# Kernel optimization log

Measured on AMD Instinct MI355X. Metric: run time of the kernel, lower is better.

Reference implementation:

```python
import jax, jax.numpy as jnp
import numpy as np
import math

B, T, D = 2, 2048, 1024
H, DH = 16, 64  # n_heads, d_head
ROPE_THETA = 10000.0


def _rope_cos_sin(seq_len, d_head, dtype):
    # inv_freq over even indices, freqs[i,j] = t_i * inv_freq_j, shape [T, d_head//2]
    inv_freq = 1.0 / (ROPE_THETA ** (jnp.arange(0, d_head, 2, dtype=jnp.float32) / d_head))
    freqs = jnp.arange(seq_len, dtype=jnp.float32)[:, None] * inv_freq[None, :]
    # emb = cat(freqs, freqs); we only ever index cos[..., :d_head//2], so keep the half
    cos = jnp.cos(freqs).astype(dtype)[None, :, None, :]  # [1,T,1,DH/2]
    sin = jnp.sin(freqs).astype(dtype)[None, :, None, :]
    return cos, sin


def _apply_rotation(x, cos, sin):
    # x: [B,T,H,DH]; rotate-half style as in the torch module
    x1, x2 = x[..., : x.shape[-1] // 2], x[..., x.shape[-1] // 2 :]
    return jnp.concatenate([x1 * cos - x2 * sin, x1 * sin + x2 * cos], axis=-1)


def setup_inputs() -> dict:
    key = jax.random.key(0)
    k1, k2, k3 = jax.random.split(key, 3)
    x = jax.random.normal(k1, (B, T, D), dtype=jnp.float32)
    # torch Linear weights stored transposed here as [in, out]; init_std=0.02
    Wqkv = jax.random.normal(k2, (D, 3 * D), dtype=jnp.float32) * 0.02
    Wout = jax.random.normal(k3, (D, D), dtype=jnp.float32) * 0.02
    return {"x": x, "Wqkv": Wqkv, "Wout": Wout}


def reference(x, Wqkv, Wout):
    b, t, d = x.shape
    qkv = x @ Wqkv  # [B,T,3D]
    q, k, v = jnp.split(qkv, 3, axis=-1)
    q = q.reshape(b, t, H, DH)
    k = k.reshape(b, t, H, DH)
    v = v.reshape(b, t, H, DH)

    cos, sin = _rope_cos_sin(t, DH, x.dtype)
    q = _apply_rotation(q, cos, sin)
    k = _apply_rotation(k, cos, sin)

    scale = 1.0 / math.sqrt(DH)
    # scores: [B,H,Tq,Tk]
    scores = jnp.einsum("bqhd,bkhd->bhqk", q, k) * scale
    causal = jnp.triu(jnp.ones((t, t), dtype=bool), k=1)
    scores = jnp.where(causal[None, None, :, :], -jnp.inf, scores)
    attn = jax.nn.softmax(scores, axis=-1)
    # dropout in eval mode -> identity
    out = jnp.einsum("bhqk,bkhd->bqhd", attn, v).reshape(b, t, d)
    return out @ Wout
```

## Files before the change

kernel.cpp:

```cpp
#include <hip/hip_runtime.h>
#include <hip/hip_bf16.h>
#include <stdint.h>
#include <math.h>

#define T_SEQ 2048
#define NHEAD 16
#define NBH   32
#define BTROW 4096

typedef __bf16 bf16_t;
typedef __bf16 bf16x4_t __attribute__((ext_vector_type(4)));
typedef __bf16 bf16x8_t __attribute__((ext_vector_type(8)));
typedef float  f32x4_t  __attribute__((ext_vector_type(4)));

#define QSCALE 0.18033688011112042f

__device__ __forceinline__ f32x4_t mfma16(bf16x8_t a, bf16x8_t b, f32x4_t c) {
  return __builtin_amdgcn_mfma_f32_16x16x32_bf16(a, b, c, 0, 0, 0);
}

__device__ __forceinline__ float fast_exp2(float x) {
#if __has_builtin(__builtin_amdgcn_exp2f)
  return __builtin_amdgcn_exp2f(x);
#else
  return exp2f(x);
#endif
}

__device__ __forceinline__ void gl_lds16(const bf16_t* g, bf16_t* l) {
  __builtin_amdgcn_global_load_lds(
      (const __attribute__((address_space(1))) void*)g,
      (__attribute__((address_space(3))) void*)l, 16, 0, 0);
}

__global__ __launch_bounds__(256) void k_cast_bf16(const float* __restrict__ in,
                                                   bf16_t* __restrict__ out, int n) {
  int tid = blockIdx.x * blockDim.x + threadIdx.x;
  int stride = gridDim.x * blockDim.x;
  for (int i = tid * 4; i < n; i += stride * 4) {
    float4 a = *(const float4*)(in + i);
    bf16x4_t r = { (bf16_t)a.x, (bf16_t)a.y, (bf16_t)a.z, (bf16_t)a.w };
    *(bf16x4_t*)(out + i) = r;
  }
}

__global__ __launch_bounds__(256) void k_trans_cast(const float* __restrict__ W,
                                                    bf16_t* __restrict__ WT,
                                                    int K, int N) {
  __shared__ float tile[32][33];
  int n0 = blockIdx.x * 32, k0 = blockIdx.y * 32;
  int tx = threadIdx.x & 31, ty = threadIdx.x >> 5;
#pragma unroll
  for (int j = 0; j < 4; j++)
    tile[ty + j * 8][tx] = W[(size_t)(k0 + ty + j * 8) * N + n0 + tx];
  __syncthreads();
#pragma unroll
  for (int j = 0; j < 4; j++)
    WT[(size_t)(n0 + ty + j * 8) * K + k0 + tx] = (bf16_t)tile[tx][ty + j * 8];
}

__global__ __launch_bounds__(256) void k_rope_table(float* __restrict__ cs,
                                                    float* __restrict__ sn) {
  int i = blockIdx.x * blockDim.x + threadIdx.x;
  if (i >= T_SEQ * 32) return;
  int t = i >> 5, j = i & 31;
  float inv = powf(10000.0f, -(float)(2 * j) / 64.0f);
  float f = (float)t * inv;
  cs[i] = cosf(f);
  sn[i] = sinf(f);
}

__global__ __launch_bounds__(256) void k_gemm_qkv(const bf16_t* __restrict__ A,
                                                  const bf16_t* __restrict__ Bt,
                                                  const float* __restrict__ cs,
                                                  const float* __restrict__ sn,
                                                  bf16_t* __restrict__ Qr,
                                                  bf16_t* __restrict__ Kr,
                                                  bf16_t* __restrict__ Vt) {
  const int K = 1024;
  __shared__ __align__(16) unsigned char smem[128 * 132 * 2];
  bf16_t* As = (bf16_t*)smem;
  bf16_t* Bs = (bf16_t*)(smem + 8192);
  bf16_t* vtile = (bf16_t*)smem;

  int m0 = blockIdx.y * 128, n0 = blockIdx.x * 128;
  int tid = threadIdx.x;
  int lane = tid & 63, w = tid >> 6;
  int wr = w >> 1, wc = w & 1;
  int l15 = lane & 15, l4 = lane >> 4;

  f32x4_t acc[4][4];
#pragma unroll
  for (int m = 0; m < 4; m++)
#pragma unroll
    for (int n = 0; n < 4; n++) acc[m][n] = (f32x4_t){0.f, 0.f, 0.f, 0.f};

  for (int k0 = 0; k0 < K; k0 += 32) {
#pragma unroll
    for (int j = 0; j < 2; j++) {
      int c = j * 256 + tid;
      int row = c >> 2, kb = c & 3;
      gl_lds16(A + (size_t)(m0 + row) * K + k0 + kb * 8, As + (size_t)(j * 256 + w * 64) * 8);
      gl_lds16(Bt + (size_t)(n0 + row) * K + k0 + kb * 8, Bs + (size_t)(j * 256 + w * 64) * 8);
    }
    __syncthreads();
    bf16x8_t af[4], bfr[4];
#pragma unroll
    for (int m = 0; m < 4; m++)
      af[m] = *(const bf16x8_t*)(As + (size_t)(wr * 64 + m * 16 + l15) * 32 + l4 * 8);
#pragma unroll
    for (int n = 0; n < 4; n++)
      bfr[n] = *(const bf16x8_t*)(Bs + (size_t)(wc * 64 + n * 16 + l15) * 32 + l4 * 8);
#pragma unroll
    for (int m = 0; m < 4; m++)
#pragma unroll
      for (int n = 0; n < 4; n++) acc[m][n] = mfma16(af[m], bfr[n], acc[m][n]);
    __syncthreads();
  }

  int region = n0 >> 10;
  if (region < 2) {
    bf16_t* dst = region ? Kr : Qr;
    float qs = region ? 1.0f : QSCALE;
    int h = ((n0 & 1023) + wc * 64) >> 6;
#pragma unroll
    for (int m = 0; m < 4; m++)
#pragma unroll
      for (int r = 0; r < 4; r++) {
        int row = m0 + wr * 64 + m * 16 + l4 * 4 + r;
        int b = row >> 11, t = row & 2047;
        size_t obase = ((size_t)(b * NHEAD + h) * T_SEQ + t) * 64;
#pragma unroll
        for (int n = 0; n < 2; n++) {
          int j = n * 16 + l15;
          float c = cs[t * 32 + j], s = sn[t * 32 + j];
          float x1 = acc[m][n][r], x2 = acc[m][n + 2][r];
          dst[obase + j]      = (bf16_t)((x1 * c - x2 * s) * qs);
          dst[obase + 32 + j] = (bf16_t)((x1 * s + x2 * c) * qs);
        }
      }
  } else {
#pragma unroll
    for (int m = 0; m < 4; m++)
#pragma unroll
      for (int n = 0; n < 4; n++)
#pragma unroll
        for (int r = 0; r < 4; r++)
          vtile[(size_t)(wc * 64 + n * 16 + l15) * 132 + wr * 64 + m * 16 + l4 * 4 + r] =
              (bf16_t)acc[m][n][r];
    __syncthreads();
    int colbase = n0 - 2048;
    int b = m0 >> 11, t0l = m0 & 2047;
#pragma unroll
    for (int p = 0; p < 64; p++) {
      int idx = p * 256 + tid;
      int dl = idx >> 7, tl = idx & 127;
      int col = colbase + dl, h = col >> 6, d = col & 63;
      Vt[((size_t)(b * NHEAD + h) * 64 + d) * T_SEQ + t0l + tl] = vtile[(size_t)dl * 132 + tl];
    }
  }
}

__global__ __launch_bounds__(256) void k_gemm2(const bf16_t* __restrict__ A,
                                               const bf16_t* __restrict__ Bt,
                                               float* __restrict__ C) {
  const int N = 1024, K = 1024;
  __shared__ __align__(16) bf16_t As[64 * 32];
  __shared__ __align__(16) bf16_t Bs[128 * 32];
  int m0 = blockIdx.y * 64, n0 = blockIdx.x * 128;
  int tid = threadIdx.x;
  int lane = tid & 63, w = tid >> 6;
  int l15 = lane & 15, l4 = lane >> 4;

  f32x4_t acc[4][2];
#pragma unroll
  for (int m = 0; m < 4; m++)
#pragma unroll
    for (int n = 0; n < 2; n++) acc[m][n] = (f32x4_t){0.f, 0.f, 0.f, 0.f};

  for (int k0 = 0; k0 < K; k0 += 32) {
    {
      int row = tid >> 2, kb = tid & 3;
      gl_lds16(A + (size_t)(m0 + row) * K + k0 + kb * 8, As + (size_t)(w * 64) * 8);
    }
#pragma unroll
    for (int j = 0; j < 2; j++) {
      int c = j * 256 + tid;
      int row = c >> 2, kb = c & 3;
      gl_lds16(Bt + (size_t)(n0 + row) * K + k0 + kb * 8, Bs + (size_t)(j * 256 + w * 64) * 8);
    }
    __syncthreads();
    bf16x8_t af[4], bfr[2];
#pragma unroll
    for (int m = 0; m < 4; m++)
      af[m] = *(const bf16x8_t*)(As + (size_t)(m * 16 + l15) * 32 + l4 * 8);
#pragma unroll
    for (int n = 0; n < 2; n++)
      bfr[n] = *(const bf16x8_t*)(Bs + (size_t)(w * 32 + n * 16 + l15) * 32 + l4 * 8);
#pragma unroll
    for (int m = 0; m < 4; m++)
#pragma unroll
      for (int n = 0; n < 2; n++) acc[m][n] = mfma16(af[m], bfr[n], acc[m][n]);
    __syncthreads();
  }
#pragma unroll
  for (int m = 0; m < 4; m++)
#pragma unroll
    for (int n = 0; n < 2; n++)
#pragma unroll
      for (int r = 0; r < 4; r++) {
        int row = m0 + m * 16 + l4 * 4 + r;
        int col = n0 + w * 32 + n * 16 + l15;
        C[(size_t)row * N + col] = acc[m][n][r];
      }
}

__global__ __launch_bounds__(256) void k_attn(const bf16_t* __restrict__ Qr,
                                              const bf16_t* __restrict__ Kr,
                                              const bf16_t* __restrict__ Vt,
                                              bf16_t* __restrict__ Ob) {
  __shared__ __align__(16) bf16_t Ks[3][64 * 64];
  __shared__ __align__(16) bf16_t Vs[3][64 * 64];
  __shared__ __align__(16) bf16_t Ps[64 * 72];
  int flat = blockIdx.x;
  int swz = (flat & 7) * 64 + (flat >> 3);
  int pidx = swz & 15, bh = swz >> 4;
  int b = bh >> 4, h = bh & 15;
  int tid = threadIdx.x, lane = tid & 63, w = tid >> 6;
  int l15 = lane & 15, l4 = lane >> 4;

  const bf16_t* Kbh = Kr + (size_t)bh * T_SEQ * 64;
  const bf16_t* Vbh = Vt + (size_t)bh * 64 * T_SEQ;

  auto stage = [&](int buf, int it) {
    int kb = it * 64;
#pragma unroll
    for (int j = 0; j < 2; j++) {
      int c = j * 256 + tid;
      int row = c >> 3, k8 = c & 7;
      int sk8 = k8 ^ (row & 7);
      gl_lds16(Kbh + (size_t)(kb + row) * 64 + sk8 * 8, Ks[buf] + (size_t)(j * 256 + w * 64) * 8);
      gl_lds16(Vbh + (size_t)row * T_SEQ + kb + sk8 * 8, Vs[buf] + (size_t)(j * 256 + w * 64) * 8);
    }
  };

  for (int pass = 0; pass < 2; pass++) {
    int qb = pass ? (31 - pidx) : pidx;
    int q0 = qb * 64;
    int nit = qb + 1;

    __builtin_amdgcn_s_barrier();

    bf16x8_t qf[2];
    size_t qbase = ((size_t)bh * T_SEQ + q0 + w * 16 + l15) * 64;
    qf[0] = *(const bf16x8_t*)(Qr + qbase + l4 * 8);
    qf[1] = *(const bf16x8_t*)(Qr + qbase + 32 + l4 * 8);

    stage(0, 0);
    if (nit > 1) stage(1, 1);

    f32x4_t o[4];
#pragma unroll
    for (int n = 0; n < 4; n++) o[n] = (f32x4_t){0.f, 0.f, 0.f, 0.f};
    float m_s = -1e30f, l_s = 0.f;

    for (int it = 0; it < nit; it++) {
      int cur = it % 3;
      if (it + 1 < nit) asm volatile("s_waitcnt vmcnt(4)" ::: "memory");
      else              asm volatile("s_waitcnt vmcnt(0)" ::: "memory");
      __builtin_amdgcn_s_barrier();
      if (it + 2 < nit) stage((it + 2) % 3, it + 2);

      f32x4_t s[4];
      __builtin_amdgcn_s_setprio(1);
#pragma unroll
      for (int n = 0; n < 4; n++) {
        int rowK = n * 16 + l15;
        const bf16_t* kp = Ks[cur] + (size_t)rowK * 64;
        int sw = rowK & 7;
        bf16x8_t kf0 = *(const bf16x8_t*)(kp + (l4 ^ sw) * 8);
        bf16x8_t kf1 = *(const bf16x8_t*)(kp + ((l4 ^ 4) ^ sw) * 8);
        s[n] = (f32x4_t){0.f, 0.f, 0.f, 0.f};
        s[n] = mfma16(kf0, qf[0], s[n]);
        s[n] = mfma16(kf1, qf[1], s[n]);
      }
      __builtin_amdgcn_s_setprio(0);

      if (it == qb) {
#pragma unroll
        for (int n = 0; n < 4; n++)
#pragma unroll
          for (int r = 0; r < 4; r++)
            if (n * 16 + l4 * 4 + r > w * 16 + l15) s[n][r] = -1e30f;
      }

      float t0 = fmaxf(fmaxf(s[0][0], s[0][1]), fmaxf(s[0][2], s[0][3]));
      float t1 = fmaxf(fmaxf(s[1][0], s[1][1]), fmaxf(s[1][2], s[1][3]));
      float t2 = fmaxf(fmaxf(s[2][0], s[2][1]), fmaxf(s[2][2], s[2][3]));
      float t3 = fmaxf(fmaxf(s[3][0], s[3][1]), fmaxf(s[3][2], s[3][3]));
      float mx = fmaxf(fmaxf(t0, t1), fmaxf(t2, t3));
      mx = fmaxf(mx, __shfl_xor(mx, 16, 64));
      mx = fmaxf(mx, __shfl_xor(mx, 32, 64));

      if (__any(mx - m_s > 8.0f)) {
        float mnew = fmaxf(m_s, mx);
        float alpha = fast_exp2(m_s - mnew);
        m_s = mnew;
        l_s *= alpha;
        float ar[4];
#pragma unroll
        for (int r = 0; r < 4; r++) ar[r] = __shfl(alpha, l4 * 4 + r, 64);
#pragma unroll
        for (int n = 0; n < 4; n++)
#pragma unroll
          for (int r = 0; r < 4; r++) o[n][r] *= ar[r];
      }

      float sum = 0.f;
#pragma unroll
      for (int n = 0; n < 4; n++) {
#pragma unroll
        for (int r = 0; r < 4; r++) s[n][r] = fast_exp2(s[n][r] - m_s);
        bf16x4_t pk = { (bf16_t)s[n][0], (bf16_t)s[n][1], (bf16_t)s[n][2], (bf16_t)s[n][3] };
        *(bf16x4_t*)(Ps + (size_t)(w * 16 + l15) * 72 + n * 16 + l4 * 4) = pk;
        sum += (s[n][0] + s[n][1]) + (s[n][2] + s[n][3]);
      }
      sum += __shfl_xor(sum, 16, 64);
      sum += __shfl_xor(sum, 32, 64);
      l_s += sum;

      __builtin_amdgcn_s_setprio(1);
#pragma unroll
      for (int ks = 0; ks < 2; ks++) {
        bf16x8_t pa = *(const bf16x8_t*)(Ps + (size_t)(w * 16 + l15) * 72 + ks * 32 + l4 * 8);
#pragma unroll
        for (int n = 0; n < 4; n++) {
          int rowV = n * 16 + l15;
          bf16x8_t vf = *(const bf16x8_t*)(Vs[cur] + (size_t)rowV * 64 +
                                           (((ks * 4 + l4) ^ (rowV & 7)) * 8));
          o[n] = mfma16(pa, vf, o[n]);
        }
      }
      __builtin_amdgcn_s_setprio(0);
    }

    float linv = 1.0f / l_s;
#pragma unroll
    for (int r = 0; r < 4; r++) {
      float ir = __shfl(linv, l4 * 4 + r, 64);
      int q = q0 + w * 16 + l4 * 4 + r;
      size_t off = ((size_t)(b * T_SEQ + q)) * 1024 + h * 64;
#pragma unroll
      for (int n = 0; n < 4; n++)
        Ob[off + n * 16 + l15] = (bf16_t)(o[n][r] * ir);
    }
  }
}

extern "C" void kernel_launch(void* const* d_in, const int* in_sizes, int n_in,
                              void* d_out, int out_size, void* d_ws, size_t ws_size,
                              hipStream_t stream) {
  const float* x    = (const float*)d_in[0];
  const float* Wqkv = (const float*)d_in[1];
  const float* Wout = (const float*)d_in[2];
  float* out = (float*)d_out;
  char* ws = (char*)d_ws;

  bf16_t* wqkvT = (bf16_t*)(ws + 0);
  bf16_t* woutT = (bf16_t*)(ws + 6291456);
  bf16_t* xb    = (bf16_t*)(ws + 8388608);
  bf16_t* Qr    = (bf16_t*)(ws + 41943040);
  bf16_t* Kr    = (bf16_t*)(ws + 50331648);
  bf16_t* Vt    = (bf16_t*)(ws + 58720256);
  float*  cs    = (float*)(ws + 67108864);
  float*  sn    = (float*)(ws + 67371008);
  bf16_t* Ob    = xb;

  k_cast_bf16<<<2048, 256, 0, stream>>>(x, xb, 4096 * 1024);
  k_trans_cast<<<dim3(3072 / 32, 1024 / 32), 256, 0, stream>>>(Wqkv, wqkvT, 1024, 3072);
  k_trans_cast<<<dim3(1024 / 32, 1024 / 32), 256, 0, stream>>>(Wout, woutT, 1024, 1024);
  k_rope_table<<<(T_SEQ * 32) / 256, 256, 0, stream>>>(cs, sn);

  k_gemm_qkv<<<dim3(3072 / 128, 4096 / 128), 256, 0, stream>>>(xb, wqkvT, cs, sn, Qr, Kr, Vt);
  k_attn<<<512, 256, 0, stream>>>(Qr, Kr, Vt, Ob);
  k_gemm2<<<dim3(1024 / 128, 4096 / 64), 256, 0, stream>>>(Ob, woutT, out);
}
```

Baseline: 119.0 us.

## Process paired query blocks concurrently in 512-thread attention blocks sharing K/V tiles

```diff
diff --git a/kernel.cpp b/kernel.cpp
--- a/kernel.cpp
+++ b/kernel.cpp
@@ -215,62 +215,62 @@
       }
 }
 
-__global__ __launch_bounds__(256) void k_attn(const bf16_t* __restrict__ Qr,
-                                              const bf16_t* __restrict__ Kr,
-                                              const bf16_t* __restrict__ Vt,
-                                              bf16_t* __restrict__ Ob) {
-  __shared__ __align__(16) bf16_t Ks[3][64 * 64];
-  __shared__ __align__(16) bf16_t Vs[3][64 * 64];
-  __shared__ __align__(16) bf16_t Ps[64 * 72];
+__global__ __launch_bounds__(512, 4) void k_attn(const bf16_t* __restrict__ Qr,
+                                                 const bf16_t* __restrict__ Kr,
+                                                 const bf16_t* __restrict__ Vt,
+                                                 bf16_t* __restrict__ Ob) {
+  __shared__ __align__(16) bf16_t Ks[2][64 * 64];
+  __shared__ __align__(16) bf16_t Vs[2][64 * 64];
+  __shared__ __align__(16) bf16_t Ps[128 * 72];
   int flat = blockIdx.x;
   int swz = (flat & 7) * 64 + (flat >> 3);
   int pidx = swz & 15, bh = swz >> 4;
   int b = bh >> 4, h = bh & 15;
   int tid = threadIdx.x, lane = tid & 63, w = tid >> 6;
+  int grp = w >> 2, wl = w & 3;
   int l15 = lane & 15, l4 = lane >> 4;
+
+  int qb = grp ? (31 - pidx) : pidx;
+  int nit = qb + 1;
+  int nit_max = 32 - pidx;
+  int q0 = qb * 64;
 
   const bf16_t* Kbh = Kr + (size_t)bh * T_SEQ * 64;
   const bf16_t* Vbh = Vt + (size_t)bh * 64 * T_SEQ;
 
+  int srow = tid >> 3;
+  int sk8 = (tid & 7) ^ (srow & 7);
+
   auto stage = [&](int buf, int it) {
     int kb = it * 64;
-#pragma unroll
-    for (int j = 0; j < 2; j++) {
-      int c = j * 256 + tid;
-      int row = c >> 3, k8 = c & 7;
-      int sk8 = k8 ^ (row & 7);
-      gl_lds16(Kbh + (size_t)(kb + row) * 64 + sk8 * 8, Ks[buf] + (size_t)(j * 256 + w * 64) * 8);
-      gl_lds16(Vbh + (size_t)row * T_SEQ + kb + sk8 * 8, Vs[buf] + (size_t)(j * 256 + w * 64) * 8);
-    }
+    gl_lds16(Kbh + (size_t)(kb + srow) * 64 + sk8 * 8, Ks[buf] + (size_t)(w * 64) * 8);
+    gl_lds16(Vbh + (size_t)srow * T_SEQ + kb + sk8 * 8, Vs[buf] + (size_t)(w * 64) * 8);
   };
 
-  for (int pass = 0; pass < 2; pass++) {
-    int qb = pass ? (31 - pidx) : pidx;
-    int q0 = qb * 64;
-    int nit = qb + 1;
-
+  bf16x8_t qf[2];
+  size_t qbase = ((size_t)bh * T_SEQ + q0 + wl * 16 + l15) * 64;
+  qf[0] = *(const bf16x8_t*)(Qr + qbase + l4 * 8);
+  qf[1] = *(const bf16x8_t*)(Qr + qbase + 32 + l4 * 8);
+
+  bf16x8_t ones;
+#pragma unroll
+  for (int i = 0; i < 8; i++) ones[i] = (bf16_t)1.0f;
+
+  f32x4_t o[4];
+#pragma unroll
+  for (int n = 0; n < 4; n++) o[n] = (f32x4_t){0.f, 0.f, 0.f, 0.f};
+  f32x4_t ls = (f32x4_t){0.f, 0.f, 0.f, 0.f};
+  float m_s = -1e30f;
+
+  stage(0, 0);
+
+  for (int it = 0; it < nit_max; it++) {
+    int cur = it & 1;
+    asm volatile("s_waitcnt vmcnt(0)" ::: "memory");
     __builtin_amdgcn_s_barrier();
-
-    bf16x8_t qf[2];
-    size_t qbase = ((size_t)bh * T_SEQ + q0 + w * 16 + l15) * 64;
-    qf[0] = *(const bf16x8_t*)(Qr + qbase + l4 * 8);
-    qf[1] = *(const bf16x8_t*)(Qr + qbase + 32 + l4 * 8);
-
-    stage(0, 0);
-    if (nit > 1) stage(1, 1);
-
-    f32x4_t o[4];
-#pragma unroll
-    for (int n = 0; n < 4; n++) o[n] = (f32x4_t){0.f, 0.f, 0.f, 0.f};
-    float m_s = -1e30f, l_s = 0.f;
-
-    for (int it = 0; it < nit; it++) {
-      int cur = it % 3;
-      if (it + 1 < nit) asm volatile("s_waitcnt vmcnt(4)" ::: "memory");
-      else              asm volatile("s_waitcnt vmcnt(0)" ::: "memory");
-      __builtin_amdgcn_s_barrier();
-      if (it + 2 < nit) stage((it + 2) % 3, it + 2);
-
+    if (it + 1 < nit_max) stage(cur ^ 1, it + 1);
+
+    if (it < nit) {
       f32x4_t s[4];
       __builtin_amdgcn_s_setprio(1);
 #pragma unroll
@@ -291,7 +291,7 @@
         for (int n = 0; n < 4; n++)
 #pragma unroll
           for (int r = 0; r < 4; r++)
-            if (n * 16 + l4 * 4 + r > w * 16 + l15) s[n][r] = -1e30f;
+            if (n * 16 + l4 * 4 + r > wl * 16 + l15) s[n][r] = -1e30f;
       }
 
       float t0 = fmaxf(fmaxf(s[0][0], s[0][1]), fmaxf(s[0][2], s[0][3]));
@@ -306,7 +306,6 @@
         float mnew = fmaxf(m_s, mx);
         float alpha = fast_exp2(m_s - mnew);
         m_s = mnew;
-        l_s *= alpha;
         float ar[4];
 #pragma unroll
         for (int r = 0; r < 4; r++) ar[r] = __shfl(alpha, l4 * 4 + r, 64);
@@ -314,25 +313,23 @@
         for (int n = 0; n < 4; n++)
 #pragma unroll
           for (int r = 0; r < 4; r++) o[n][r] *= ar[r];
-      }
-
-      float sum = 0.f;
+#pragma unroll
+        for (int r = 0; r < 4; r++) ls[r] *= ar[r];
+      }
+
 #pragma unroll
       for (int n = 0; n < 4; n++) {
 #pragma unroll
         for (int r = 0; r < 4; r++) s[n][r] = fast_exp2(s[n][r] - m_s);
         bf16x4_t pk = { (bf16_t)s[n][0], (bf16_t)s[n][1], (bf16_t)s[n][2], (bf16_t)s[n][3] };
         *(bf16x4_t*)(Ps + (size_t)(w * 16 + l15) * 72 + n * 16 + l4 * 4) = pk;
-        sum += (s[n][0] + s[n][1]) + (s[n][2] + s[n][3]);
-      }
-      sum += __shfl_xor(sum, 16, 64);
-      sum += __shfl_xor(sum, 32, 64);
-      l_s += sum;
+      }
 
       __builtin_amdgcn_s_setprio(1);
 #pragma unroll
       for (int ks = 0; ks < 2; ks++) {
         bf16x8_t pa = *(const bf16x8_t*)(Ps + (size_t)(w * 16 + l15) * 72 + ks * 32 + l4 * 8);
+        ls = mfma16(pa, ones, ls);
 #pragma unroll
         for (int n = 0; n < 4; n++) {
           int rowV = n * 16 + l15;
@@ -343,17 +340,16 @@
       }
       __builtin_amdgcn_s_setprio(0);
     }
-
-    float linv = 1.0f / l_s;
-#pragma unroll
-    for (int r = 0; r < 4; r++) {
-      float ir = __shfl(linv, l4 * 4 + r, 64);
-      int q = q0 + w * 16 + l4 * 4 + r;
-      size_t off = ((size_t)(b * T_SEQ + q)) * 1024 + h * 64;
-#pragma unroll
-      for (int n = 0; n < 4; n++)
-        Ob[off + n * 16 + l15] = (bf16_t)(o[n][r] * ir);
-    }
+  }
+
+#pragma unroll
+  for (int r = 0; r < 4; r++) {
+    float ir = 1.0f / ls[r];
+    int q = q0 + wl * 16 + l4 * 4 + r;
+    size_t off = ((size_t)(b * T_SEQ + q)) * 1024 + h * 64;
+#pragma unroll
+    for (int n = 0; n < 4; n++)
+      Ob[off + n * 16 + l15] = (bf16_t)(o[n][r] * ir);
   }
 }
 
@@ -382,6 +378,6 @@
   k_rope_table<<<(T_SEQ * 32) / 256, 256, 0, stream>>>(cs, sn);
 
   k_gemm_qkv<<<dim3(3072 / 128, 4096 / 128), 256, 0, stream>>>(xb, wqkvT, cs, sn, Qr, Kr, Vt);
-  k_attn<<<512, 256, 0, stream>>>(Qr, Kr, Vt, Ob);
+  k_attn<<<512, 512, 0, stream>>>(Qr, Kr, Vt, Ob);
   k_gemm2<<<dim3(1024 / 128, 4096 / 64), 256, 0, stream>>>(Ob, woutT, out);
 }
```

After: 116.6 us. 1.02x faster.
